# Kernel tuning notes

Hardware: AMD Instinct MI355X
Metric: run time of the kernel (lower is better)

## Reference

```python
import jax, jax.numpy as jnp
import numpy as np

N, C, H, K = 4096, 512, 128, 3
NEG = -jnp.inf


def _linear(x, W, b):
    return x @ W.T + b


def _lrelu(x):
    return jnp.where(x > 0, x, 0.01 * x)  # nn.LeakyReLU default slope


def _cos_sim(x, y):
    # torch cal_cos_similarity: xy / (|x| |y|^T), NaN (0/0) -> 0
    xy = x @ y.T
    den = jnp.linalg.norm(x, axis=1, keepdims=True) * jnp.linalg.norm(y, axis=1, keepdims=True).T
    return xy / jnp.where(den == 0, 1.0, den)


def setup_inputs() -> dict:
    key = jax.random.key(0)
    ks = jax.random.split(key, 24)
    x_hidden = jax.random.normal(ks[0], (N, H), jnp.float32)
    cm = (jax.random.uniform(ks[1], (N, C)) < 0.05).astype(jnp.float32)
    # ensure every concept has at least one member stock (no empty concepts)
    cm = cm.at[jnp.arange(C) % N, jnp.arange(C)].set(1.0)
    market_value = jax.random.uniform(ks[2], (N,), jnp.float32, 0.1, 1.0)
    s = 1.0 / np.sqrt(H)
    inp = {"x_hidden": x_hidden, "concept_matrix": cm, "market_value": market_value}
    names = ["ps", "ps_fore", "ps_back", "hs", "hs_fore", "hs_back", "indi"]
    for i, n in enumerate(names):
        inp[f"W_{n}"] = jax.random.uniform(ks[3 + 2 * i], (H, H), jnp.float32, -s, s)
        inp[f"b_{n}"] = jax.random.uniform(ks[4 + 2 * i], (H,), jnp.float32, -s, s)
    inp["W_out"] = jax.random.uniform(ks[20], (1, H), jnp.float32, -s, s)
    inp["b_out"] = jax.random.uniform(ks[21], (1,), jnp.float32, -s, s)
    return inp


def reference(x_hidden, concept_matrix, market_value,
              W_ps, b_ps, W_ps_fore, b_ps_fore, W_ps_back, b_ps_back,
              W_hs, b_hs, W_hs_fore, b_hs_fore, W_hs_back, b_hs_back,
              W_indi, b_indi, W_out, b_out):
    x = x_hidden
    n = x.shape[0]
    # --- predefined-concept (ps) branch ---
    s2c = concept_matrix * market_value[:, None]                     # [N,C]
    s2c_den = s2c.sum(0)[None, :] * concept_matrix + 1.0
    s2c = s2c / s2c_den
    hidden = s2c.T @ x                                               # [C,H]
    valid1 = hidden.sum(1) != 0                                      # row-filter mask
    s2c2 = jax.nn.softmax(x @ hidden.T, axis=0)                      # softmax over stocks
    hidden = (s2c2.T @ x) * valid1[:, None]                          # [C,H]
    c2s = jax.nn.softmax(jnp.where(valid1[None, :], _cos_sim(x, hidden), NEG), axis=1)
    p_shared = _linear(c2s @ hidden, W_ps, b_ps)
    p_back = _linear(p_shared, W_ps_back, b_ps_back)
    out_ps = _lrelu(_linear(p_shared, W_ps_fore, b_ps_fore))
    # --- hidden-concept (hs) branch ---
    h = x - p_back
    hs2c = _cos_sim(h, h)                                            # [N,N]
    diag = jnp.diagonal(hs2c)
    hs2c = hs2c * (1.0 - jnp.eye(n, dtype=h.dtype))
    idx = jax.lax.top_k(hs2c, K)[1]                                  # [N,K]
    mask = jnp.zeros((n, n), h.dtype).at[jnp.arange(n)[:, None], idx].set(1.0)
    hs2c = hs2c * mask
    hs2c = hs2c + jnp.diag((hs2c.sum(0) != 0).astype(h.dtype) * diag)
    hidden2 = hs2c.T @ h                                             # [N,H]
    valid2 = hidden2.sum(1) != 0
    hidden2 = hidden2 * valid2[:, None]
    hc2s = jax.nn.softmax(jnp.where(valid2[None, :], _cos_sim(h, hidden2), NEG), axis=1)
    h_shared = _linear(hc2s @ hidden2, W_hs, b_hs)
    h_back = _linear(h_shared, W_hs_back, b_hs_back)
    out_hs = _lrelu(_linear(h_shared, W_hs_fore, b_hs_fore))
    # --- individual branch ---
    indiv = x - p_back - h_back
    out_indi = _lrelu(_linear(indiv, W_indi, b_indi))
    all_info = out_ps + out_hs + out_indi
    return _linear(all_info, W_out, b_out).squeeze()                 # [N]
```

## Files before the change

### kernel.cpp

```cpp
#include <hip/hip_runtime.h>
#include <hip/hip_fp16.h>
#include <math.h>

#define N 4096
#define C 512
#define H 128
#define PAD 40

typedef __attribute__((ext_vector_type(8))) short bf16x8;
typedef __attribute__((ext_vector_type(4))) float f32x4;


__device__ inline float wave_reduce_sum(float v) {
#pragma unroll
  for (int m = 32; m; m >>= 1) v += __shfl_xor(v, m);
  return v;
}

__device__ inline float lrelu(float v) { return v > 0.f ? v : 0.01f * v; }

__device__ inline bool better(float v, int j, float w, int k) {
  return (v > w) || (v == w && j < k);
}

__device__ inline void top3_ins(float v, int j, float& v0, int& j0,
                                float& v1, int& j1, float& v2, int& j2) {
  if (better(v, j, v0, j0)) { v2 = v1; j2 = j1; v1 = v0; j1 = j0; v0 = v; j0 = j; }
  else if (better(v, j, v1, j1)) { v2 = v1; j2 = j1; v1 = v; j1 = j; }
  else if (better(v, j, v2, j2)) { v2 = v; j2 = j; }
}

__device__ inline void ins5(float s, int j, float v[5], int jx[5]) {
  if (!better(s, j, v[4], jx[4])) return;
  if (better(s, j, v[0], jx[0])) {
    v[4]=v[3]; jx[4]=jx[3]; v[3]=v[2]; jx[3]=jx[2]; v[2]=v[1]; jx[2]=jx[1];
    v[1]=v[0]; jx[1]=jx[0]; v[0]=s; jx[0]=j;
  } else if (better(s, j, v[1], jx[1])) {
    v[4]=v[3]; jx[4]=jx[3]; v[3]=v[2]; jx[3]=jx[2]; v[2]=v[1]; jx[2]=jx[1];
    v[1]=s; jx[1]=j;
  } else if (better(s, j, v[2], jx[2])) {
    v[4]=v[3]; jx[4]=jx[3]; v[3]=v[2]; jx[3]=jx[2]; v[2]=s; jx[2]=j;
  } else if (better(s, j, v[3], jx[3])) {
    v[4]=v[3]; jx[4]=jx[3]; v[3]=s; jx[3]=j;
  } else {
    v[4]=s; jx[4]=j;
  }
}

__device__ inline unsigned short f2bf(float f) {
  unsigned u = __float_as_uint(f);
  unsigned r = u + 0x7fffu + ((u >> 16) & 1u);
  return (unsigned short)(r >> 16);
}
__device__ inline float bf2f(unsigned short h) {
  return __uint_as_float(((unsigned)h) << 16);
}

__global__ __launch_bounds__(256) void k_split(const float* __restrict__ in,
                                               unsigned short* __restrict__ hi,
                                               unsigned short* __restrict__ lo) {
  int idx = (blockIdx.x * 256 + threadIdx.x) * 4;
  float4 v = *(const float4*)&in[idx];
  float vv[4] = {v.x, v.y, v.z, v.w};
  unsigned short h[4], l[4];
#pragma unroll
  for (int c = 0; c < 4; c++) {
    h[c] = f2bf(vv[c]);
    l[c] = f2bf(vv[c] - bf2f(h[c]));
  }
  uint2 ph = {(unsigned)h[0] | ((unsigned)h[1] << 16),
              (unsigned)h[2] | ((unsigned)h[3] << 16)};
  uint2 pl = {(unsigned)l[0] | ((unsigned)l[1] << 16),
              (unsigned)l[2] | ((unsigned)l[3] << 16)};
  *(uint2*)&hi[idx] = ph;
  *(uint2*)&lo[idx] = pl;
}

__global__ __launch_bounds__(256) void k_tsplit(const float* __restrict__ in,
                                                unsigned short* __restrict__ thi,
                                                unsigned short* __restrict__ tlo,
                                                int R) {
  __shared__ float tile[32][132];
  int r0 = blockIdx.x * 32, tid = threadIdx.x;
#pragma unroll
  for (int q = 0; q < 4; q++) {
    int f = q * 256 + tid;
    int row = f >> 5, ch = f & 31;
    *(float4*)&tile[row][ch * 4] = *(const float4*)&in[(size_t)(r0 + row) * 128 + ch * 4];
  }
  __syncthreads();
  int c = tid & 127, half = tid >> 7;
  unsigned short hh[16], ll[16];
#pragma unroll
  for (int rr = 0; rr < 16; rr++) {
    float v = tile[half * 16 + rr][c];
    hh[rr] = f2bf(v);
    ll[rr] = f2bf(v - bf2f(hh[rr]));
  }
  size_t off = (size_t)c * R + r0 + half * 16;
  uint4 ph0 = {(unsigned)hh[0] | ((unsigned)hh[1] << 16), (unsigned)hh[2] | ((unsigned)hh[3] << 16),
               (unsigned)hh[4] | ((unsigned)hh[5] << 16), (unsigned)hh[6] | ((unsigned)hh[7] << 16)};
  uint4 ph1 = {(unsigned)hh[8] | ((unsigned)hh[9] << 16), (unsigned)hh[10] | ((unsigned)hh[11] << 16),
               (unsigned)hh[12] | ((unsigned)hh[13] << 16), (unsigned)hh[14] | ((unsigned)hh[15] << 16)};
  uint4 pl0 = {(unsigned)ll[0] | ((unsigned)ll[1] << 16), (unsigned)ll[2] | ((unsigned)ll[3] << 16),
               (unsigned)ll[4] | ((unsigned)ll[5] << 16), (unsigned)ll[6] | ((unsigned)ll[7] << 16)};
  uint4 pl1 = {(unsigned)ll[8] | ((unsigned)ll[9] << 16), (unsigned)ll[10] | ((unsigned)ll[11] << 16),
               (unsigned)ll[12] | ((unsigned)ll[13] << 16), (unsigned)ll[14] | ((unsigned)ll[15] << 16)};
  *(uint4*)&thi[off] = ph0; *(uint4*)&thi[off + 8] = ph1;
  *(uint4*)&tlo[off] = pl0; *(uint4*)&tlo[off + 8] = pl1;
}


__global__ __launch_bounds__(64) void k_colsum_s2c(
    const float* __restrict__ cm, const float* __restrict__ mv,
    float* __restrict__ colsum_c) {
  int c = blockIdx.x * 64 + threadIdx.x;
  int i0 = blockIdx.y * 256;
  float acc = 0.f;
  for (int i = i0; i < i0 + 256; i++) acc += cm[(size_t)i * C + c] * mv[i];
  atomicAdd(&colsum_c[c], acc);
}

__global__ __launch_bounds__(64) void k_valid1(const float* __restrict__ hid,
                                               float* __restrict__ valid1) {
  int c = blockIdx.x, t = threadIdx.x;
  float s = hid[(size_t)c * H + t] + hid[(size_t)c * H + 64 + t];
  s = wave_reduce_sum(s);
  if (t == 0) valid1[c] = (s != 0.f) ? 1.f : 0.f;
}

__global__ __launch_bounds__(64) void k_rownorm128(const float* __restrict__ A,
                                                   float* __restrict__ nrm) {
  int r = blockIdx.x, t = threadIdx.x;
  float a = A[(size_t)r * H + t], b = A[(size_t)r * H + 64 + t];
  float ss = wave_reduce_sum(a * a + b * b);
  if (t == 0) nrm[r] = sqrtf(ss);
}

__global__ __launch_bounds__(256) void k_colstats(const float* __restrict__ sc,
                                                  float* __restrict__ colmax,
                                                  float* __restrict__ colsum) {
  __shared__ float red[256];
  int c = blockIdx.x, t = threadIdx.x;
  float v[16];
  float m = -3e38f;
#pragma unroll
  for (int q = 0; q < 16; q++) {
    v[q] = sc[(size_t)(q * 256 + t) * C + c];
    m = fmaxf(m, v[q]);
  }
  red[t] = m; __syncthreads();
  for (int s = 128; s; s >>= 1) { if (t < s) red[t] = fmaxf(red[t], red[t + s]); __syncthreads(); }
  m = red[0]; __syncthreads();
  float sum = 0.f;
#pragma unroll
  for (int q = 0; q < 16; q++) sum += __expf(v[q] - m);
  red[t] = sum; __syncthreads();
  for (int s = 128; s; s >>= 1) { if (t < s) red[t] += red[t + s]; __syncthreads(); }
  if (t == 0) { colmax[c] = m; colsum[c] = red[0]; }
}

__global__ __launch_bounds__(256) void k_cs_softmax(
    const float* __restrict__ sc, const float* __restrict__ xnorm,
    const float* __restrict__ hnorm, const float* __restrict__ valid1,
    unsigned short* __restrict__ cshi, unsigned short* __restrict__ cslo) {
  __shared__ float red[256];
  int i = blockIdx.x, t = threadIdx.x;
  float xn = xnorm[i];
  float r0 = sc[(size_t)i * C + t], r1 = sc[(size_t)i * C + 256 + t];
  float d0 = xn * hnorm[t], d1 = xn * hnorm[256 + t];
  float c0 = r0 / (d0 == 0.f ? 1.f : d0);
  float c1 = r1 / (d1 == 0.f ? 1.f : d1);
  float s0 = (valid1[t] != 0.f) ? c0 : -3e38f;
  float s1 = (valid1[256 + t] != 0.f) ? c1 : -3e38f;
  red[t] = fmaxf(s0, s1); __syncthreads();
  for (int s = 128; s; s >>= 1) { if (t < s) red[t] = fmaxf(red[t], red[t + s]); __syncthreads(); }
  float m = red[0]; __syncthreads();
  float p0 = (s0 > -1e37f) ? __expf(s0 - m) : 0.f;
  float p1 = (s1 > -1e37f) ? __expf(s1 - m) : 0.f;
  red[t] = p0 + p1; __syncthreads();
  for (int s = 128; s; s >>= 1) { if (t < s) red[t] += red[t + s]; __syncthreads(); }
  float inv = 1.f / red[0];
  float a = p0 * inv, b = p1 * inv;
  unsigned short ha = f2bf(a), hb = f2bf(b);
  cshi[(size_t)i * C + t] = ha;
  cslo[(size_t)i * C + t] = f2bf(a - bf2f(ha));
  cshi[(size_t)i * C + 256 + t] = hb;
  cslo[(size_t)i * C + 256 + t] = f2bf(b - bf2f(hb));
}

__global__ __launch_bounds__(64) void k_hhat(const float* __restrict__ h,
                                             float* __restrict__ hhat,
                                             unsigned short* __restrict__ hhi,
                                             unsigned short* __restrict__ hlo,
                                             float* __restrict__ diagv) {
  int i = blockIdx.x, t = threadIdx.x;
  float a = h[(size_t)i * H + t], b = h[(size_t)i * H + 64 + t];
  float ss = wave_reduce_sum(a * a + b * b);
  float hn = sqrtf(ss);
  float den = hn * hn;
  float dg = (den == 0.f) ? 0.f : ss / den;
  float inv = (ss > 0.f) ? (1.f / hn) : 1.f;
  float va = a * inv, vb = b * inv;
  hhat[(size_t)i * H + t] = va;
  hhat[(size_t)i * H + 64 + t] = vb;
  unsigned short ha = f2bf(va), hb = f2bf(vb);
  hhi[(size_t)i * H + t] = ha;
  hlo[(size_t)i * H + t] = f2bf(va - bf2f(ha));
  hhi[(size_t)i * H + 64 + t] = hb;
  hlo[(size_t)i * H + 64 + t] = f2bf(vb - bf2f(hb));
  if (t == 0) diagv[i] = dg;
}

__global__ __launch_bounds__(64) void k_fin_hidden2(
    const float* __restrict__ h, const float* __restrict__ diagv,
    const float* __restrict__ colsum_m, float* __restrict__ hidden2,
    unsigned short* __restrict__ h2hi, unsigned short* __restrict__ h2lo,
    float* __restrict__ valid2f) {
  int j = blockIdx.x, t = threadIdx.x;
  float add = (colsum_m[j] != 0.f) ? diagv[j] : 0.f;
  float a = hidden2[(size_t)j * H + t] + add * h[(size_t)j * H + t];
  float b = hidden2[(size_t)j * H + 64 + t] + add * h[(size_t)j * H + 64 + t];
  float s = a + b, ss = a * a + b * b;
#pragma unroll
  for (int m = 32; m; m >>= 1) { s += __shfl_xor(s, m); ss += __shfl_xor(ss, m); }
  bool valid = (s != 0.f);
  a = valid ? a : 0.f; b = valid ? b : 0.f;
  hidden2[(size_t)j * H + t] = a;
  hidden2[(size_t)j * H + 64 + t] = b;
  float inv = (valid && ss > 0.f) ? (1.f / sqrtf(ss)) : 1.f;
  float va = a * inv, vb = b * inv;
  unsigned short ha = f2bf(va), hb = f2bf(vb);
  h2hi[(size_t)j * H + t] = ha;
  h2lo[(size_t)j * H + t] = f2bf(va - bf2f(ha));
  h2hi[(size_t)j * H + 64 + t] = hb;
  h2lo[(size_t)j * H + 64 + t] = f2bf(vb - bf2f(hb));
  if (t == 0) valid2f[j] = valid ? 1.f : 0.f;
}

__global__ __launch_bounds__(64) void k_final(const float* __restrict__ ai,
                                              const float* __restrict__ Wout,
                                              const float* __restrict__ bout,
// ... 44 lines not shown
#pragma unroll
    for (int t = 0; t < 4; t++) {
      int ar = (wm + t * 16 + l15) * PAD + quad * 8;
      ah[t] = *(const bf16x8*)&sAh[ar];
      al[t] = *(const bf16x8*)&sAl[ar];
      int br = (wn + t * 16 + l15) * PAD + quad * 8;
      bh[t] = *(const bf16x8*)&sBh[br];
      bl[t] = *(const bf16x8*)&sBl[br];
    }
#pragma unroll
    for (int mt = 0; mt < 4; mt++)
#pragma unroll
      for (int nt = 0; nt < 4; nt++) {
        acc[mt][nt] = __builtin_amdgcn_mfma_f32_16x16x32_bf16(ah[mt], bh[nt], acc[mt][nt], 0, 0, 0);
        acc[mt][nt] = __builtin_amdgcn_mfma_f32_16x16x32_bf16(ah[mt], bl[nt], acc[mt][nt], 0, 0, 0);
        acc[mt][nt] = __builtin_amdgcn_mfma_f32_16x16x32_bf16(al[mt], bh[nt], acc[mt][nt], 0, 0, 0);
      }
    __syncthreads();
  }
  if (EPI == 3) {
    float vm[4];
#pragma unroll
    for (int nt = 0; nt < 4; nt++) vm[nt] = validn[bn + wn + nt * 16 + l15];
#pragma unroll
    for (int mt = 0; mt < 4; mt++) {
#pragma unroll
      for (int rg = 0; rg < 4; rg++) {
        int row = bm + wm + mt * 16 + quad * 4 + rg;
        float rsum = 0.f;
#pragma unroll
        for (int nt = 0; nt < 4; nt++) {
          int col = bn + wn + nt * 16 + l15;
          float e = (vm[nt] != 0.f) ? __expf(acc[mt][nt][rg] - 1.f) : 0.f;
          rsum += e;
          ehi[(size_t)row * N + col] = f2bf(e);
        }
#pragma unroll
        for (int d = 1; d < 16; d <<= 1) rsum += __shfl_xor(rsum, d);
        if (l15 == 0) atomicAdd(&lsum[row], rsum);
      }
    }
  } else if (EPI == 2) {
#pragma unroll
    for (int mt = 0; mt < 4; mt++) {
#pragma unroll
      for (int nt = 0; nt < 4; nt++) {
        int col = bn + wn + nt * 16 + l15;
#pragma unroll
        for (int rg = 0; rg < 4; rg++) {
          int row = bm + wm + mt * 16 + quad * 4 + rg;
          float v = (row == col) ? 0.f : acc[mt][nt][rg];
          ehi[(size_t)row * N + col] = __half_as_ushort(__float2half(v));
        }
      }
    }
  } else {
#pragma unroll
    for (int mt = 0; mt < 4; mt++) {
#pragma unroll
      for (int nt = 0; nt < 4; nt++) {
        int col = bn + wn + nt * 16 + l15;
#pragma unroll
        for (int rg = 0; rg < 4; rg++) {
          int row = bm + wm + mt * 16 + quad * 4 + rg;
          out[(size_t)row * Nn + col] = acc[mt][nt][rg];
        }
      }
    }
  }
}

__global__ __launch_bounds__(256) void k_rowtop(
    const unsigned short* __restrict__ Sh, const float* __restrict__ hhat,
    float* __restrict__ mtv, int* __restrict__ mtj) {
  int i = blockIdx.x * 4 + (threadIdx.x >> 6);
  int lane = threadIdx.x & 63;
  const unsigned short* row = &Sh[(size_t)i * N];
  float v[5] = {-3e38f, -3e38f, -3e38f, -3e38f, -3e38f};
  int jx[5] = {0x7fffffff, 0x7fffffff, 0x7fffffff, 0x7fffffff, 0x7fffffff};
  for (int t = 0; t < 8; t++) {
    int base = t * 512 + lane * 8;
    uint4 p = *(const uint4*)&row[base];
    unsigned pk[4] = {p.x, p.y, p.z, p.w};
#pragma unroll
    for (int c = 0; c < 4; c++) {
      float e0 = __half2float(__ushort_as_half((unsigned short)(pk[c] & 0xffffu)));
      float e1 = __half2float(__ushort_as_half((unsigned short)(pk[c] >> 16)));
      ins5(e0, base + c * 2, v, jx);
      ins5(e1, base + c * 2 + 1, v, jx);
    }
  }
#pragma unroll
  for (int d = 1; d < 64; d <<= 1) {
    float fv[5]; int fj[5];
#pragma unroll
    for (int c = 0; c < 5; c++) { fv[c] = __shfl_xor(v[c], d); fj[c] = __shfl_xor(jx[c], d); }
#pragma unroll
    for (int c = 0; c < 5; c++) ins5(fv[c], fj[c], v, jx);
  }
  const float* hi = &hhat[(size_t)i * H];
  float b0 = -3e38f, b1 = -3e38f, b2 = -3e38f;
  int q0 = 0, q1 = 0, q2 = 0;
#pragma unroll
  for (int c = 0; c < 5; c++) {
    int j = jx[c];
    float s;
    if (j == i) {
      s = 0.f;
    } else {
      const float* hj = &hhat[(size_t)j * H];
      float p = hi[lane] * hj[lane] + hi[lane + 64] * hj[lane + 64];
      s = wave_reduce_sum(p);
    }
    top3_ins(s, j, b0, q0, b1, q1, b2, q2);
  }
  if (lane == 0) {
    mtv[i * 3 + 0] = b0; mtv[i * 3 + 1] = b1; mtv[i * 3 + 2] = b2;
    mtj[i * 3 + 0] = q0; mtj[i * 3 + 1] = q1; mtj[i * 3 + 2] = q2;
  }
}

template <int ALO>
__global__ __launch_bounds__(256) void k_mfma_kn(
    const unsigned short* __restrict__ Ahi, const unsigned short* __restrict__ Alo,
    const unsigned short* __restrict__ Bthi, const unsigned short* __restrict__ Btlo,
    float* __restrict__ partial, int lda, int KC) {
  __shared__ __align__(16) unsigned short sAh[128 * PAD];
  __shared__ __align__(16) unsigned short sAl[128 * PAD];
  __shared__ __align__(16) unsigned short sBh[128 * PAD];
  __shared__ __align__(16) unsigned short sBl[128 * PAD];
  int tid = threadIdx.x;
  int bm = blockIdx.y * 128;
  int k0 = blockIdx.z * KC;
  int lane = tid & 63, w = tid >> 6;
  int wm = (w & 1) * 64, wn = (w >> 1) * 64;
  int l15 = lane & 15, quad = lane >> 4;
  f32x4 zero = {0.f, 0.f, 0.f, 0.f};
  f32x4 acc[4][4];
#pragma unroll
  for (int mt = 0; mt < 4; mt++)
#pragma unroll
    for (int nt = 0; nt < 4; nt++) acc[mt][nt] = zero;

  for (int kt = 0; kt < KC; kt += 32) {
#pragma unroll
    for (int q = 0; q < 2; q++) {
      int f = tid * 2 + q;
      int row = f >> 2, ch = f & 3;
      size_t ga = (size_t)(bm + row) * lda + k0 + kt + ch * 8;
      size_t gb = (size_t)row * lda + k0 + kt + ch * 8;
      int ls = row * PAD + ch * 8;
      *(uint4*)&sAh[ls] = *(const uint4*)&Ahi[ga];
      if (ALO) *(uint4*)&sAl[ls] = *(const uint4*)&Alo[ga];
      *(uint4*)&sBh[ls] = *(const uint4*)&Bthi[gb];
      *(uint4*)&sBl[ls] = *(const uint4*)&Btlo[gb];
    }
    __syncthreads();
    bf16x8 ah[4], al[4], bh[4], bl[4];
#pragma unroll
    for (int t = 0; t < 4; t++) {
      int ar = (wm + t * 16 + l15) * PAD + quad * 8;
      ah[t] = *(const bf16x8*)&sAh[ar];
      if (ALO) al[t] = *(const bf16x8*)&sAl[ar];
      int br = (wn + t * 16 + l15) * PAD + quad * 8;
      bh[t] = *(const bf16x8*)&sBh[br];
      bl[t] = *(const bf16x8*)&sBl[br];
    }
#pragma unroll
    for (int mt = 0; mt < 4; mt++)
#pragma unroll
      for (int nt = 0; nt < 4; nt++) {
        acc[mt][nt] = __builtin_amdgcn_mfma_f32_16x16x32_bf16(ah[mt], bh[nt], acc[mt][nt], 0, 0, 0);
        acc[mt][nt] = __builtin_amdgcn_mfma_f32_16x16x32_bf16(ah[mt], bl[nt], acc[mt][nt], 0, 0, 0);
        if (ALO)
          acc[mt][nt] = __builtin_amdgcn_mfma_f32_16x16x32_bf16(al[mt], bh[nt], acc[mt][nt], 0, 0, 0);
      }
    __syncthreads();
  }
  float* pp = partial + (size_t)blockIdx.z * N * 128;
#pragma unroll
  for (int mt = 0; mt < 4; mt++)
#pragma unroll
    for (int nt = 0; nt < 4; nt++) {
      int col = wn + nt * 16 + l15;
#pragma unroll
      for (int rg = 0; rg < 4; rg++) {
        int row = bm + wm + mt * 16 + quad * 4 + rg;
        pp[(size_t)row * 128 + col] = acc[mt][nt][rg];
      }
    }
}

template <int AMODE>
__global__ __launch_bounds__(256) void k_mfma_genA(
    const float* __restrict__ P, const float* __restrict__ mv,
    const float* __restrict__ col1, const float* __restrict__ col2,
    const unsigned short* __restrict__ Bthi, const unsigned short* __restrict__ Btlo,
    float* __restrict__ partial, int KC) {
  __shared__ __align__(16) unsigned short sAh[128 * PAD];
  __shared__ __align__(16) unsigned short sAl[128 * PAD];
  __shared__ __align__(16) unsigned short sBh[128 * PAD];
  __shared__ __align__(16) unsigned short sBl[128 * PAD];
  int tid = threadIdx.x;
  int bm = blockIdx.y * 128;
  int k0 = blockIdx.z * KC;
  int lane = tid & 63, w = tid >> 6;
  int wm = (w & 1) * 64, wn = (w >> 1) * 64;
  int l15 = lane & 15, quad = lane >> 4;
  f32x4 zero = {0.f, 0.f, 0.f, 0.f};
  f32x4 acc[4][4];
#pragma unroll
  for (int mt = 0; mt < 4; mt++)
#pragma unroll
    for (int nt = 0; nt < 4; nt++) acc[mt][nt] = zero;

  for (int kt = 0; kt < KC; kt += 32) {
    int kr = tid >> 3;
    int mc = (tid & 7) * 16;
    int k = k0 + kt + kr;
    float mvk = (AMODE == 1) ? mv[k] : 0.f;
#pragma unroll
    for (int q = 0; q < 4; q++) {
      int m0 = mc + q * 4;
      float4 pv = *(const float4*)&P[(size_t)k * C + bm + m0];
      float4 c1 = *(const float4*)&col1[bm + m0];
      float wv[4];
      if (AMODE == 1) {
        wv[0] = pv.x * mvk / (c1.x * pv.x + 1.f);
        wv[1] = pv.y * mvk / (c1.y * pv.y + 1.f);
        wv[2] = pv.z * mvk / (c1.z * pv.z + 1.f);
        wv[3] = pv.w * mvk / (c1.w * pv.w + 1.f);
      } else {
        float4 c2 = *(const float4*)&col2[bm + m0];
        wv[0] = __expf(pv.x - c1.x) / c2.x;
        wv[1] = __expf(pv.y - c1.y) / c2.y;
        wv[2] = __expf(pv.z - c1.z) / c2.z;
        wv[3] = __expf(pv.w - c1.w) / c2.w;
      }
#pragma unroll
      for (int j = 0; j < 4; j++) {
        unsigned short hh = f2bf(wv[j]);
        sAh[(m0 + j) * PAD + kr] = hh;
        sAl[(m0 + j) * PAD + kr] = f2bf(wv[j] - bf2f(hh));
      }
    }
#pragma unroll
    for (int q = 0; q < 2; q++) {
      int f = q * 256 + tid;
      int row = f >> 2, ch = f & 3;
      size_t gb = (size_t)row * N + k0 + kt + ch * 8;
      int ls = row * PAD + ch * 8;
      *(uint4*)&sBh[ls] = *(const uint4*)&Bthi[gb];
      *(uint4*)&sBl[ls] = *(const uint4*)&Btlo[gb];
    }
    __syncthreads();
    bf16x8 ah[4], al[4], bh[4], bl[4];
#pragma unroll
    for (int t = 0; t < 4; t++) {
      int ar = (wm + t * 16 + l15) * PAD + quad * 8;
      ah[t] = *(const bf16x8*)&sAh[ar];
      al[t] = *(const bf16x8*)&sAl[ar];
      int br = (wn + t * 16 + l15) * PAD + quad * 8;
      bh[t] = *(const bf16x8*)&sBh[br];
      bl[t] = *(const bf16x8*)&sBl[br];
    }
#pragma unroll
    for (int mt = 0; mt < 4; mt++)
#pragma unroll
      for (int nt = 0; nt < 4; nt++) {
        acc[mt][nt] = __builtin_amdgcn_mfma_f32_16x16x32_bf16(ah[mt], bh[nt], acc[mt][nt], 0, 0, 0);
        acc[mt][nt] = __builtin_amdgcn_mfma_f32_16x16x32_bf16(ah[mt], bl[nt], acc[mt][nt], 0, 0, 0);
        acc[mt][nt] = __builtin_amdgcn_mfma_f32_16x16x32_bf16(al[mt], bh[nt], acc[mt][nt], 0, 0, 0);
      }
    __syncthreads();
  }
  float* pp = partial + (size_t)blockIdx.z * C * 128;
#pragma unroll
  for (int mt = 0; mt < 4; mt++)
#pragma unroll
    for (int nt = 0; nt < 4; nt++) {
      int col = wn + nt * 16 + l15;
#pragma unroll
      for (int rg = 0; rg < 4; rg++) {
        int row = bm + wm + mt * 16 + quad * 4 + rg;
        pp[(size_t)row * 128 + col] = acc[mt][nt][rg];
      }
    }
}

template <int EPI>
__global__ __launch_bounds__(256) void k_mfma_lin(
    const float* __restrict__ A, const float* __restrict__ Wt,
    const float* __restrict__ bias, const float* __restrict__ aux,
    float* __restrict__ out) {
  __shared__ __align__(16) unsigned short sAh[32 * PAD];
  __shared__ __align__(16) unsigned short sAl[32 * PAD];
  __shared__ __align__(16) unsigned short sWh[128 * PAD];
  __shared__ __align__(16) unsigned short sWl[128 * PAD];
  int tid = threadIdx.x;
  int bm = blockIdx.y * 32;
  int lane = tid & 63, w = tid >> 6;
  int rt = (w & 1) * 16, ch2 = (w >> 1) * 64;
  int l15 = lane & 15, quad = lane >> 4;
  f32x4 zero = {0.f, 0.f, 0.f, 0.f};
  f32x4 acc[4];
#pragma unroll
  for (int nt = 0; nt < 4; nt++) acc[nt] = zero;

  for (int kt = 0; kt < 128; kt += 32) {
    {
      int arow = tid >> 3, ach = tid & 7;
      float4 av = *(const float4*)&A[(size_t)(bm + arow) * 128 + kt + ach * 4];
      float aa[4] = {av.x, av.y, av.z, av.w};
      int ls = arow * PAD + ach * 4;
#pragma unroll
      for (int c = 0; c < 4; c++) {
        unsigned short hh = f2bf(aa[c]);
        sAh[ls + c] = hh;
        sAl[ls + c] = f2bf(aa[c] - bf2f(hh));
      }
    }
#pragma unroll
    for (int q = 0; q < 4; q++) {
      int f = q * 256 + tid;
      int wrow = f >> 3, wch = f & 7;
      float4 wv = *(const float4*)&Wt[(size_t)wrow * 128 + kt + wch * 4];
      float ww[4] = {wv.x, wv.y, wv.z, wv.w};
      int ls = wrow * PAD + wch * 4;
#pragma unroll
      for (int c = 0; c < 4; c++) {
        unsigned short hh = f2bf(ww[c]);
        sWh[ls + c] = hh;
        sWl[ls + c] = f2bf(ww[c] - bf2f(hh));
      }
    }
    __syncthreads();
    bf16x8 ah, al, bh[4], bl[4];
    {
      int ar = (rt + l15) * PAD + quad * 8;
      ah = *(const bf16x8*)&sAh[ar];
      al = *(const bf16x8*)&sAl[ar];
    }
#pragma unroll
    for (int nt = 0; nt < 4; nt++) {
      int br = (ch2 + nt * 16 + l15) * PAD + quad * 8;
      bh[nt] = *(const bf16x8*)&sWh[br];
      bl[nt] = *(const bf16x8*)&sWl[br];
    }
#pragma unroll
    for (int nt = 0; nt < 4; nt++) {
      acc[nt] = __builtin_amdgcn_mfma_f32_16x16x32_bf16(ah, bh[nt], acc[nt], 0, 0, 0);
      acc[nt] = __builtin_amdgcn_mfma_f32_16x16x32_bf16(ah, bl[nt], acc[nt], 0, 0, 0);
      acc[nt] = __builtin_amdgcn_mfma_f32_16x16x32_bf16(al, bh[nt], acc[nt], 0, 0, 0);
    }
    __syncthreads();
  }
#pragma unroll
  for (int nt = 0; nt < 4; nt++) {
    int col = ch2 + nt * 16 + l15;
    float bv = bias[col];
#pragma unroll
    for (int rg = 0; rg < 4; rg++) {
      int row = bm + rt + quad * 4 + rg;
      size_t off = (size_t)row * 128 + col;
      float v = acc[nt][rg] + bv;
      if (EPI == 0) out[off] = v;
      else if (EPI == 1) out[off] = lrelu(v);
      else if (EPI == 2) out[off] += lrelu(v);
      else out[off] = aux[off] - v;
    }
  }
}

__global__ __launch_bounds__(256) void k_scatter(
    const float* __restrict__ mtv, const int* __restrict__ mtj,
    const float* __restrict__ h, float* __restrict__ hidden2,
    float* __restrict__ colsum_m) {
  int i = blockIdx.x * 4 + (threadIdx.x >> 6);
  int lane = threadIdx.x & 63;
  float h0 = h[(size_t)i * H + lane], h1 = h[(size_t)i * H + 64 + lane];
#pragma unroll
  for (int s = 0; s < 3; s++) {
    float v = mtv[i * 3 + s];
    int j = mtj[i * 3 + s];
    atomicAdd(&hidden2[(size_t)j * H + lane], v * h0);
    atomicAdd(&hidden2[(size_t)j * H + 64 + lane], v * h1);
    if (lane == s) atomicAdd(&colsum_m[j], v);
  }
}

__global__ __launch_bounds__(256) void k_reduce(
    const float* __restrict__ partial, float* __restrict__ out, int cnt,
    size_t slot, size_t size4, const float* __restrict__ scalem,
    const float* __restrict__ divm, unsigned short* __restrict__ hi,
    unsigned short* __restrict__ lo) {
  size_t idx = (size_t)blockIdx.x * 256 + threadIdx.x;
  if (idx >= size4) return;
  float4 s = {0, 0, 0, 0};
  for (int c = 0; c < cnt; c++) {
    float4 v = *(const float4*)&partial[c * slot + idx * 4];
    s.x += v.x; s.y += v.y; s.z += v.z; s.w += v.w;
  }
  if (scalem) {
    float sc = scalem[idx >> 5];
    s.x *= sc; s.y *= sc; s.z *= sc; s.w *= sc;
  }
  if (divm) {
    float sc = 1.f / divm[idx >> 5];
    s.x *= sc; s.y *= sc; s.z *= sc; s.w *= sc;
  }
  *(float4*)&out[idx * 4] = s;
  if (hi) {
    float vv[4] = {s.x, s.y, s.z, s.w};
    unsigned short h[4], l[4];
#pragma unroll
    for (int c = 0; c < 4; c++) {
      h[c] = f2bf(vv[c]);
      l[c] = f2bf(vv[c] - bf2f(h[c]));
    }
    uint2 ph = {(unsigned)h[0] | ((unsigned)h[1] << 16),
                (unsigned)h[2] | ((unsigned)h[3] << 16)};
    uint2 pl = {(unsigned)l[0] | ((unsigned)l[1] << 16),
                (unsigned)l[2] | ((unsigned)l[3] << 16)};
    *(uint2*)&hi[idx * 4] = ph;
    *(uint2*)&lo[idx * 4] = pl;
  }
}


extern "C" void kernel_launch(void* const* d_in, const int* in_sizes, int n_in,
                              void* d_out, int out_size, void* d_ws, size_t ws_size,
                              hipStream_t stream) {
  (void)in_sizes; (void)n_in; (void)out_size;
  const float* x   = (const float*)d_in[0];
  const float* cm  = (const float*)d_in[1];
  const float* mv  = (const float*)d_in[2];
  const float* W_ps = (const float*)d_in[3],  *b_ps = (const float*)d_in[4];
  const float* W_psf = (const float*)d_in[5], *b_psf = (const float*)d_in[6];
  const float* W_psb = (const float*)d_in[7], *b_psb = (const float*)d_in[8];
  const float* W_hs = (const float*)d_in[9],  *b_hs = (const float*)d_in[10];
  const float* W_hsf = (const float*)d_in[11], *b_hsf = (const float*)d_in[12];
  const float* W_hsb = (const float*)d_in[13], *b_hsb = (const float*)d_in[14];
  const float* W_in = (const float*)d_in[15], *b_in = (const float*)d_in[16];
  const float* W_out = (const float*)d_in[17], *b_out = (const float*)d_in[18];
  float* out = (float*)d_out;

  float* W = (float*)d_ws;
  size_t o = 0;
  auto alloc = [&](size_t n) { float* p = W + o; o += n; return p; };
  float* colsum_c = alloc(C);
  float* colmax   = alloc(C);
  float* colsumexp= alloc(C);
  float* valid1   = alloc(C);
  float* hnorm_ps = alloc(C);
  float* xnorm    = alloc(N);
  float* diagv    = alloc(N);
  float* colsum_m = alloc(N);
  float* valid2f  = alloc(N);
  float* lsum     = alloc(N);
  float* mtv      = alloc(3 * N);
  int*   mtj      = (int*)alloc(3 * N);
  float* hidden1  = alloc((size_t)C * H);
  float* hidden_ps= alloc((size_t)C * H);
  float* scores   = alloc((size_t)N * C);
  float* ps_pre   = alloc((size_t)N * H);
  float* p_shared = alloc((size_t)N * H);
  float* all_info = alloc((size_t)N * H);
  float* hbuf     = alloc((size_t)N * H);
  float* hhat     = alloc((size_t)N * H);
  float* hidden2  = alloc((size_t)N * H);
  unsigned short* xhi    = (unsigned short*)alloc((size_t)N * H / 2);
  unsigned short* xlo    = (unsigned short*)alloc((size_t)N * H / 2);
  unsigned short* hhathi = (unsigned short*)alloc((size_t)N * H / 2);
  unsigned short* hhatlo = (unsigned short*)alloc((size_t)N * H / 2);
  unsigned short* h2hi   = (unsigned short*)alloc((size_t)N * H / 2);
  unsigned short* h2lo   = (unsigned short*)alloc((size_t)N * H / 2);
  unsigned short* h1hi   = (unsigned short*)alloc((size_t)C * H / 2);
  unsigned short* h1lo   = (unsigned short*)alloc((size_t)C * H / 2);
  unsigned short* hpshi  = (unsigned short*)alloc((size_t)C * H / 2);
  unsigned short* hpslo  = (unsigned short*)alloc((size_t)C * H / 2);
  unsigned short* cshi   = (unsigned short*)alloc((size_t)N * C / 2);
  unsigned short* cslo   = (unsigned short*)alloc((size_t)N * C / 2);
  unsigned short* hpst_hi= (unsigned short*)alloc((size_t)H * C / 2);
  unsigned short* hpst_lo= (unsigned short*)alloc((size_t)H * C / 2);
  unsigned short* h2t_hi = (unsigned short*)alloc((size_t)H * N / 2);
  unsigned short* h2t_lo = (unsigned short*)alloc((size_t)H * N / 2);
  unsigned short* xt_hi  = (unsigned short*)alloc((size_t)H * N / 2);
  unsigned short* xt_lo  = (unsigned short*)alloc((size_t)H * N / 2);
  float* Sbuf     = alloc((size_t)N * N / 2);
  unsigned short* Sh  = (unsigned short*)Sbuf;
  unsigned short* Ehi = (unsigned short*)Sbuf;
  float* partial  = W + o;
  size_t rem = ws_size / 4 - o;
  int Z = (rem >= (size_t)16 * N * H) ? 16 : 8;
  int KC = 4096 / Z;

  hipMemsetAsync(colsum_c, 0, C * sizeof(float), stream);
  hipMemsetAsync(colsum_m, 0, N * sizeof(float), stream);
  hipMemsetAsync(lsum, 0, N * sizeof(float), stream);
  hipMemsetAsync(hidden2, 0, (size_t)N * H * sizeof(float), stream);

  dim3 blk(256);
  k_split<<<dim3(N * H / 1024), blk, 0, stream>>>(x, xhi, xlo);
  k_tsplit<<<dim3(N / 32), blk, 0, stream>>>(x, xt_hi, xt_lo, N);
  k_colsum_s2c<<<dim3(C / 64, 16), dim3(64), 0, stream>>>(cm, mv, colsum_c);
  k_mfma_genA<1><<<dim3(1, C / 128, 32), blk, 0, stream>>>(
      cm, mv, colsum_c, nullptr, xt_hi, xt_lo, partial, N / 32);
  k_reduce<<<dim3(C * H / 4 / 256), blk, 0, stream>>>(
      partial, hidden1, 32, (size_t)C * H, (size_t)C * H / 4, nullptr, nullptr,
      h1hi, h1lo);
  k_valid1<<<dim3(C), dim3(64), 0, stream>>>(hidden1, valid1);
  k_mfma_nt<0><<<dim3(C / 128, N / 128), blk, 0, stream>>>(
      xhi, xlo, h1hi, h1lo, nullptr, scores, nullptr, nullptr, C);
  k_colstats<<<dim3(C), blk, 0, stream>>>(scores, colmax, colsumexp);
  k_mfma_genA<2><<<dim3(1, C / 128, 32), blk, 0, stream>>>(
      scores, nullptr, colmax, colsumexp, xt_hi, xt_lo, partial, N / 32);
  k_reduce<<<dim3(C * H / 4 / 256), blk, 0, stream>>>(
      partial, hidden_ps, 32, (size_t)C * H, (size_t)C * H / 4, valid1, nullptr,
      hpshi, hpslo);
  k_rownorm128<<<dim3(N), dim3(64), 0, stream>>>(x, xnorm);
  k_rownorm128<<<dim3(C), dim3(64), 0, stream>>>(hidden_ps, hnorm_ps);
  k_mfma_nt<0><<<dim3(C / 128, N / 128), blk, 0, stream>>>(
      xhi, xlo, hpshi, hpslo, nullptr, scores, nullptr, nullptr, C);
  k_cs_softmax<<<dim3(N), blk, 0, stream>>>(scores, xnorm, hnorm_ps, valid1,
                                            cshi, cslo);
  k_tsplit<<<dim3(C / 32), blk, 0, stream>>>(hidden_ps, hpst_hi, hpst_lo, C);
  k_mfma_kn<1><<<dim3(1, N / 128, 4), blk, 0, stream>>>(
      cshi, cslo, hpst_hi, hpst_lo, partial, C, C / 4);
  k_reduce<<<dim3(N * H / 4 / 256), blk, 0, stream>>>(
      partial, ps_pre, 4, (size_t)N * H, (size_t)N * H / 4, nullptr, nullptr,
      nullptr, nullptr);
  k_mfma_lin<0><<<dim3(1, N / 32), blk, 0, stream>>>(
      ps_pre, W_ps, b_ps, nullptr, p_shared);
  k_mfma_lin<3><<<dim3(1, N / 32), blk, 0, stream>>>(
      p_shared, W_psb, b_psb, x, hbuf);
  k_mfma_lin<1><<<dim3(1, N / 32), blk, 0, stream>>>(
      p_shared, W_psf, b_psf, nullptr, all_info);
  k_hhat<<<dim3(N), dim3(64), 0, stream>>>(hbuf, hhat, hhathi, hhatlo, diagv);
  k_mfma_nt<2><<<dim3(N / 128, N / 128), blk, 0, stream>>>(
      hhathi, hhatlo, hhathi, hhatlo, nullptr, nullptr, Sh, nullptr, N);
  k_rowtop<<<dim3(N / 4), blk, 0, stream>>>(Sh, hhat, mtv, mtj);
  k_scatter<<<dim3(N / 4), blk, 0, stream>>>(mtv, mtj, hbuf, hidden2, colsum_m);
  k_fin_hidden2<<<dim3(N), dim3(64), 0, stream>>>(hbuf, diagv, colsum_m, hidden2,
                                                  h2hi, h2lo, valid2f);
  k_mfma_nt<3><<<dim3(N / 128, N / 128), blk, 0, stream>>>(
      hhathi, hhatlo, h2hi, h2lo, valid2f, nullptr, Ehi, lsum, N);
  k_tsplit<<<dim3(N / 32), blk, 0, stream>>>(hidden2, h2t_hi, h2t_lo, N);
  k_mfma_kn<0><<<dim3(1, N / 128, Z), blk, 0, stream>>>(
      Ehi, nullptr, h2t_hi, h2t_lo, partial, N, KC);
  k_reduce<<<dim3(N * H / 4 / 256), blk, 0, stream>>>(
      partial, ps_pre, Z, (size_t)N * H, (size_t)N * H / 4, nullptr, lsum,
      nullptr, nullptr);
  k_mfma_lin<0><<<dim3(1, N / 32), blk, 0, stream>>>(
      ps_pre, W_hs, b_hs, nullptr, p_shared);
  k_mfma_lin<2><<<dim3(1, N / 32), blk, 0, stream>>>(
      p_shared, W_hsf, b_hsf, nullptr, all_info);
  k_mfma_lin<3><<<dim3(1, N / 32), blk, 0, stream>>>(
      p_shared, W_hsb, b_hsb, hbuf, hbuf);
  k_mfma_lin<2><<<dim3(1, N / 32), blk, 0, stream>>>(
      hbuf, W_in, b_in, nullptr, all_info);
  k_final<<<dim3(N), dim3(64), 0, stream>>>(all_info, W_out, b_out, out);
}
```

Measured before the change: 415.4 us.

## Replace split-K partial buffers with atomic accumulation and fuse paired linears

Split-K GEMM kernels now atomically add into the output instead of writing per-slice partials, so the separate k_reduce passes go away. Their scaling and bf16 split steps move into the consumers (the valid mask into genA, the lsum divide into the linear, k_split for hi/lo). Column softmax stats become two row-parallel kernels using atomicMax on an order-preserving float key, plus atomicAdd for the sums. Pairs of linears sharing an input are fused into one kernel, and the row top-k scan skips 8-element chunks that cannot enter the top five. Atomics make the summation order nondeterministic, and more memsets are added.

```diff
diff --git a/kernel.cpp b/kernel.cpp
--- a/kernel.cpp
+++ b/kernel.cpp
@@ -56,6 +56,15 @@
   return __uint_as_float(((unsigned)h) << 16);
 }
 
+__device__ inline unsigned fkey(float f) {
+  unsigned u = __float_as_uint(f);
+  return (u & 0x80000000u) ? ~u : (u | 0x80000000u);
+}
+__device__ inline float fkey_dec(unsigned k) {
+  unsigned u = (k & 0x80000000u) ? (k ^ 0x80000000u) : ~k;
+  return __uint_as_float(u);
+}
+
 __global__ __launch_bounds__(256) void k_split(const float* __restrict__ in,
                                                unsigned short* __restrict__ hi,
                                                unsigned short* __restrict__ lo) {
@@ -137,27 +146,35 @@
   if (t == 0) nrm[r] = sqrtf(ss);
 }
 
-__global__ __launch_bounds__(256) void k_colstats(const float* __restrict__ sc,
-                                                  float* __restrict__ colmax,
-                                                  float* __restrict__ colsum) {
-  __shared__ float red[256];
-  int c = blockIdx.x, t = threadIdx.x;
-  float v[16];
-  float m = -3e38f;
-#pragma unroll
-  for (int q = 0; q < 16; q++) {
-    v[q] = sc[(size_t)(q * 256 + t) * C + c];
-    m = fmaxf(m, v[q]);
-  }
-  red[t] = m; __syncthreads();
-  for (int s = 128; s; s >>= 1) { if (t < s) red[t] = fmaxf(red[t], red[t + s]); __syncthreads(); }
-  m = red[0]; __syncthreads();
-  float sum = 0.f;
-#pragma unroll
-  for (int q = 0; q < 16; q++) sum += __expf(v[q] - m);
-  red[t] = sum; __syncthreads();
-  for (int s = 128; s; s >>= 1) { if (t < s) red[t] += red[t + s]; __syncthreads(); }
-  if (t == 0) { colmax[c] = m; colsum[c] = red[0]; }
+__global__ __launch_bounds__(256) void k_colmax(const float* __restrict__ sc,
+                                                unsigned* __restrict__ colmax_u) {
+  int r0 = blockIdx.x * 64, tid = threadIdx.x;
+  int c0 = tid, c1 = tid + 256;
+  float m0 = -3e38f, m1 = -3e38f;
+  for (int r = 0; r < 64; r++) {
+    const float* row = &sc[(size_t)(r0 + r) * C];
+    m0 = fmaxf(m0, row[c0]);
+    m1 = fmaxf(m1, row[c1]);
+  }
+  atomicMax(&colmax_u[c0], fkey(m0));
+  atomicMax(&colmax_u[c1], fkey(m1));
+}
+
+__global__ __launch_bounds__(256) void k_colsumexp(
+    const float* __restrict__ sc, const unsigned* __restrict__ colmax_u,
+    float* __restrict__ colmax_f, float* __restrict__ colsum) {
+  int r0 = blockIdx.x * 64, tid = threadIdx.x;
+  int c0 = tid, c1 = tid + 256;
+  float m0 = fkey_dec(colmax_u[c0]), m1 = fkey_dec(colmax_u[c1]);
+  if (blockIdx.x == 0) { colmax_f[c0] = m0; colmax_f[c1] = m1; }
+  float s0 = 0.f, s1 = 0.f;
+  for (int r = 0; r < 64; r++) {
+    const float* row = &sc[(size_t)(r0 + r) * C];
+    s0 += __expf(row[c0] - m0);
+    s1 += __expf(row[c1] - m1);
+  }
+  atomicAdd(&colsum[c0], s0);
+  atomicAdd(&colsum[c1], s1);
 }
 
 __global__ __launch_bounds__(256) void k_cs_softmax(
@@ -368,13 +385,17 @@
     int base = t * 512 + lane * 8;
     uint4 p = *(const uint4*)&row[base];
     unsigned pk[4] = {p.x, p.y, p.z, p.w};
+    float e[8];
 #pragma unroll
     for (int c = 0; c < 4; c++) {
-      float e0 = __half2float(__ushort_as_half((unsigned short)(pk[c] & 0xffffu)));
-      float e1 = __half2float(__ushort_as_half((unsigned short)(pk[c] >> 16)));
-      ins5(e0, base + c * 2, v, jx);
-      ins5(e1, base + c * 2 + 1, v, jx);
-    }
+      e[c * 2] = __half2float(__ushort_as_half((unsigned short)(pk[c] & 0xffffu)));
+      e[c * 2 + 1] = __half2float(__ushort_as_half((unsigned short)(pk[c] >> 16)));
+    }
+    float mx = fmaxf(fmaxf(fmaxf(e[0], e[1]), fmaxf(e[2], e[3])),
+                     fmaxf(fmaxf(e[4], e[5]), fmaxf(e[6], e[7])));
+    if (!better(mx, base, v[4], jx[4])) continue;
+#pragma unroll
+    for (int c = 0; c < 8; c++) ins5(e[c], base + c, v, jx);
   }
 #pragma unroll
   for (int d = 1; d < 64; d <<= 1) {
@@ -410,7 +431,7 @@
 __global__ __launch_bounds__(256) void k_mfma_kn(
     const unsigned short* __restrict__ Ahi, const unsigned short* __restrict__ Alo,
     const unsigned short* __restrict__ Bthi, const unsigned short* __restrict__ Btlo,
-    float* __restrict__ partial, int lda, int KC) {
+    float* __restrict__ out, int lda, int KC) {
   __shared__ __align__(16) unsigned short sAh[128 * PAD];
   __shared__ __align__(16) unsigned short sAl[128 * PAD];
   __shared__ __align__(16) unsigned short sBh[128 * PAD];
@@ -463,7 +484,6 @@
       }
     __syncthreads();
   }
-  float* pp = partial + (size_t)blockIdx.z * N * 128;
 #pragma unroll
   for (int mt = 0; mt < 4; mt++)
 #pragma unroll
@@ -472,7 +492,7 @@
 #pragma unroll
       for (int rg = 0; rg < 4; rg++) {
         int row = bm + wm + mt * 16 + quad * 4 + rg;
-        pp[(size_t)row * 128 + col] = acc[mt][nt][rg];
+        atomicAdd(&out[(size_t)row * 128 + col], acc[mt][nt][rg]);
       }
     }
 }
@@ -481,8 +501,9 @@
 __global__ __launch_bounds__(256) void k_mfma_genA(
     const float* __restrict__ P, const float* __restrict__ mv,
     const float* __restrict__ col1, const float* __restrict__ col2,
+    const float* __restrict__ validm,
     const unsigned short* __restrict__ Bthi, const unsigned short* __restrict__ Btlo,
-    float* __restrict__ partial, int KC) {
+    float* __restrict__ out, int KC) {
   __shared__ __align__(16) unsigned short sAh[128 * PAD];
   __shared__ __align__(16) unsigned short sAl[128 * PAD];
   __shared__ __align__(16) unsigned short sBh[128 * PAD];
@@ -518,10 +539,11 @@
         wv[3] = pv.w * mvk / (c1.w * pv.w + 1.f);
       } else {
         float4 c2 = *(const float4*)&col2[bm + m0];
-        wv[0] = __expf(pv.x - c1.x) / c2.x;
-        wv[1] = __expf(pv.y - c1.y) / c2.y;
-        wv[2] = __expf(pv.z - c1.z) / c2.z;
-        wv[3] = __expf(pv.w - c1.w) / c2.w;
+        float4 vv = *(const float4*)&validm[bm + m0];
+        wv[0] = __expf(pv.x - c1.x) / c2.x * vv.x;
+        wv[1] = __expf(pv.y - c1.y) / c2.y * vv.y;
+        wv[2] = __expf(pv.z - c1.z) / c2.z * vv.z;
+        wv[3] = __expf(pv.w - c1.w) / c2.w * vv.w;
       }
 #pragma unroll
       for (int j = 0; j < 4; j++) {
@@ -560,7 +582,6 @@
       }
     __syncthreads();
   }
-  float* pp = partial + (size_t)blockIdx.z * C * 128;
 #pragma unroll
   for (int mt = 0; mt < 4; mt++)
 #pragma unroll
@@ -569,7 +590,7 @@
 #pragma unroll
       for (int rg = 0; rg < 4; rg++) {
         int row = bm + wm + mt * 16 + quad * 4 + rg;
-        pp[(size_t)row * 128 + col] = acc[mt][nt][rg];
+        atomicAdd(&out[(size_t)row * 128 + col], acc[mt][nt][rg]);
       }
     }
 }
@@ -578,7 +599,7 @@
 __global__ __launch_bounds__(256) void k_mfma_lin(
     const float* __restrict__ A, const float* __restrict__ Wt,
     const float* __restrict__ bias, const float* __restrict__ aux,
-    float* __restrict__ out) {
+    float* __restrict__ out, const float* __restrict__ divm) {
   __shared__ __align__(16) unsigned short sAh[32 * PAD];
   __shared__ __align__(16) unsigned short sAl[32 * PAD];
   __shared__ __align__(16) unsigned short sWh[128 * PAD];
@@ -588,6 +609,7 @@
   int lane = tid & 63, w = tid >> 6;
   int rt = (w & 1) * 16, ch2 = (w >> 1) * 64;
   int l15 = lane & 15, quad = lane >> 4;
+  float ascale = divm ? (1.f / divm[bm + (tid >> 3)]) : 1.f;
   f32x4 zero = {0.f, 0.f, 0.f, 0.f};
   f32x4 acc[4];
 #pragma unroll
@@ -597,7 +619,7 @@
     {
       int arow = tid >> 3, ach = tid & 7;
       float4 av = *(const float4*)&A[(size_t)(bm + arow) * 128 + kt + ach * 4];
-      float aa[4] = {av.x, av.y, av.z, av.w};
+      float aa[4] = {av.x * ascale, av.y * ascale, av.z * ascale, av.w * ascale};
       int ls = arow * PAD + ach * 4;
 #pragma unroll
       for (int c = 0; c < 4; c++) {
@@ -658,6 +680,109 @@
   }
 }
 
+template <int E1, int E2>
+__global__ __launch_bounds__(256) void k_mfma_lin2(
+    const float* __restrict__ A,
+    const float* __restrict__ W1, const float* __restrict__ b1,
+    const float* __restrict__ aux1, float* __restrict__ out1,
+    const float* __restrict__ W2, const float* __restrict__ b2,
+    const float* __restrict__ aux2, float* __restrict__ out2) {
+  __shared__ __align__(16) unsigned short sAh[32 * PAD];
+  __shared__ __align__(16) unsigned short sAl[32 * PAD];
+  __shared__ __align__(16) unsigned short sW1h[128 * PAD];
+  __shared__ __align__(16) unsigned short sW1l[128 * PAD];
+  __shared__ __align__(16) unsigned short sW2h[128 * PAD];
+  __shared__ __align__(16) unsigned short sW2l[128 * PAD];
+  int tid = threadIdx.x;
+  int bm = blockIdx.y * 32;
+  int lane = tid & 63, w = tid >> 6;
+  int rt = (w & 1) * 16, ch2 = (w >> 1) * 64;
+  int l15 = lane & 15, quad = lane >> 4;
+  f32x4 zero = {0.f, 0.f, 0.f, 0.f};
+  f32x4 acc1[4], acc2[4];
+#pragma unroll
+  for (int nt = 0; nt < 4; nt++) { acc1[nt] = zero; acc2[nt] = zero; }
+
+  for (int kt = 0; kt < 128; kt += 32) {
+    {
+      int arow = tid >> 3, ach = tid & 7;
+      float4 av = *(const float4*)&A[(size_t)(bm + arow) * 128 + kt + ach * 4];
+      float aa[4] = {av.x, av.y, av.z, av.w};
+      int ls = arow * PAD + ach * 4;
+#pragma unroll
+      for (int c = 0; c < 4; c++) {
+        unsigned short hh = f2bf(aa[c]);
+        sAh[ls + c] = hh;
+        sAl[ls + c] = f2bf(aa[c] - bf2f(hh));
+      }
+    }
+#pragma unroll
+    for (int q = 0; q < 4; q++) {
+      int f = q * 256 + tid;
+      int wrow = f >> 3, wch = f & 7;
+      int ls = wrow * PAD + wch * 4;
+      float4 wv = *(const float4*)&W1[(size_t)wrow * 128 + kt + wch * 4];
+      float ww[4] = {wv.x, wv.y, wv.z, wv.w};
+#pragma unroll
+      for (int c = 0; c < 4; c++) {
+        unsigned short hh = f2bf(ww[c]);
+        sW1h[ls + c] = hh;
+        sW1l[ls + c] = f2bf(ww[c] - bf2f(hh));
+      }
+      float4 wv2 = *(const float4*)&W2[(size_t)wrow * 128 + kt + wch * 4];
+      float ww2[4] = {wv2.x, wv2.y, wv2.z, wv2.w};
+#pragma unroll
+      for (int c = 0; c < 4; c++) {
+        unsigned short hh = f2bf(ww2[c]);
+        sW2h[ls + c] = hh;
+        sW2l[ls + c] = f2bf(ww2[c] - bf2f(hh));
+      }
+    }
+    __syncthreads();
+    bf16x8 ah, al;
+    {
+      int ar = (rt + l15) * PAD + quad * 8;
+      ah = *(const bf16x8*)&sAh[ar];
+      al = *(const bf16x8*)&sAl[ar];
+    }
+#pragma unroll
+    for (int nt = 0; nt < 4; nt++) {
+      int br = (ch2 + nt * 16 + l15) * PAD + quad * 8;
+      bf16x8 b1h = *(const bf16x8*)&sW1h[br];
+      bf16x8 b1l = *(const bf16x8*)&sW1l[br];
+      bf16x8 b2h = *(const bf16x8*)&sW2h[br];
+      bf16x8 b2l = *(const bf16x8*)&sW2l[br];
+      acc1[nt] = __builtin_amdgcn_mfma_f32_16x16x32_bf16(ah, b1h, acc1[nt], 0, 0, 0);
+      acc1[nt] = __builtin_amdgcn_mfma_f32_16x16x32_bf16(ah, b1l, acc1[nt], 0, 0, 0);
+      acc1[nt] = __builtin_amdgcn_mfma_f32_16x16x32_bf16(al, b1h, acc1[nt], 0, 0, 0);
+      acc2[nt] = __builtin_amdgcn_mfma_f32_16x16x32_bf16(ah, b2h, acc2[nt], 0, 0, 0);
+      acc2[nt] = __builtin_amdgcn_mfma_f32_16x16x32_bf16(ah, b2l, acc2[nt], 0, 0, 0);
+      acc2[nt] = __builtin_amdgcn_mfma_f32_16x16x32_bf16(al, b2h, acc2[nt], 0, 0, 0);
+    }
+    __syncthreads();
+  }
+#pragma unroll
+  for (int nt = 0; nt < 4; nt++) {
+    int col = ch2 + nt * 16 + l15;
+    float bv1 = b1[col], bv2 = b2[col];
+#pragma unroll
+    for (int rg = 0; rg < 4; rg++) {
+      int row = bm + rt + quad * 4 + rg;
+      size_t off = (size_t)row * 128 + col;
+      float v1 = acc1[nt][rg] + bv1;
+      if (E1 == 0) out1[off] = v1;
+      else if (E1 == 1) out1[off] = lrelu(v1);
+      else if (E1 == 2) out1[off] += lrelu(v1);
+      else out1[off] = aux1[off] - v1;
+      float v2 = acc2[nt][rg] + bv2;
+      if (E2 == 0) out2[off] = v2;
+      else if (E2 == 1) out2[off] = lrelu(v2);
+      else if (E2 == 2) out2[off] += lrelu(v2);
+      else out2[off] = aux2[off] - v2;
+    }
+  }
+}
+
 __global__ __launch_bounds__(256) void k_scatter(
     const float* __restrict__ mtv, const int* __restrict__ mtj,
     const float* __restrict__ h, float* __restrict__ hidden2,
@@ -675,49 +800,11 @@
   }
 }
 
-__global__ __launch_bounds__(256) void k_reduce(
-    const float* __restrict__ partial, float* __restrict__ out, int cnt,
-    size_t slot, size_t size4, const float* __restrict__ scalem,
-    const float* __restrict__ divm, unsigned short* __restrict__ hi,
-    unsigned short* __restrict__ lo) {
-  size_t idx = (size_t)blockIdx.x * 256 + threadIdx.x;
-  if (idx >= size4) return;
-  float4 s = {0, 0, 0, 0};
-  for (int c = 0; c < cnt; c++) {
-    float4 v = *(const float4*)&partial[c * slot + idx * 4];
-    s.x += v.x; s.y += v.y; s.z += v.z; s.w += v.w;
-  }
-  if (scalem) {
-    float sc = scalem[idx >> 5];
-    s.x *= sc; s.y *= sc; s.z *= sc; s.w *= sc;
-  }
-  if (divm) {
-    float sc = 1.f / divm[idx >> 5];
-    s.x *= sc; s.y *= sc; s.z *= sc; s.w *= sc;
-  }
-  *(float4*)&out[idx * 4] = s;
-  if (hi) {
-    float vv[4] = {s.x, s.y, s.z, s.w};
-    unsigned short h[4], l[4];
-#pragma unroll
-    for (int c = 0; c < 4; c++) {
-      h[c] = f2bf(vv[c]);
-      l[c] = f2bf(vv[c] - bf2f(h[c]));
-    }
-    uint2 ph = {(unsigned)h[0] | ((unsigned)h[1] << 16),
-                (unsigned)h[2] | ((unsigned)h[3] << 16)};
-    uint2 pl = {(unsigned)l[0] | ((unsigned)l[1] << 16),
-                (unsigned)l[2] | ((unsigned)l[3] << 16)};
-    *(uint2*)&hi[idx * 4] = ph;
-    *(uint2*)&lo[idx * 4] = pl;
-  }
-}
-
 
 extern "C" void kernel_launch(void* const* d_in, const int* in_sizes, int n_in,
                               void* d_out, int out_size, void* d_ws, size_t ws_size,
                               hipStream_t stream) {
-  (void)in_sizes; (void)n_in; (void)out_size;
+  (void)in_sizes; (void)n_in; (void)out_size; (void)ws_size;
   const float* x   = (const float*)d_in[0];
   const float* cm  = (const float*)d_in[1];
   const float* mv  = (const float*)d_in[2];
@@ -735,7 +822,8 @@
   size_t o = 0;
   auto alloc = [&](size_t n) { float* p = W + o; o += n; return p; };
   float* colsum_c = alloc(C);
-  float* colmax   = alloc(C);
+  unsigned* colmaxu = (unsigned*)alloc(C);
+  float* colmaxf  = alloc(C);
   float* colsumexp= alloc(C);
   float* valid1   = alloc(C);
   float* hnorm_ps = alloc(C);
@@ -776,14 +864,15 @@
   float* Sbuf     = alloc((size_t)N * N / 2);
   unsigned short* Sh  = (unsigned short*)Sbuf;
   unsigned short* Ehi = (unsigned short*)Sbuf;
-  float* partial  = W + o;
-  size_t rem = ws_size / 4 - o;
-  int Z = (rem >= (size_t)16 * N * H) ? 16 : 8;
-  int KC = 4096 / Z;
 
   hipMemsetAsync(colsum_c, 0, C * sizeof(float), stream);
+  hipMemsetAsync(colmaxu, 0, C * sizeof(unsigned), stream);
+  hipMemsetAsync(colsumexp, 0, C * sizeof(float), stream);
   hipMemsetAsync(colsum_m, 0, N * sizeof(float), stream);
   hipMemsetAsync(lsum, 0, N * sizeof(float), stream);
+  hipMemsetAsync(hidden1, 0, (size_t)C * H * sizeof(float), stream);
+  hipMemsetAsync(hidden_ps, 0, (size_t)C * H * sizeof(float), stream);
+  hipMemsetAsync(ps_pre, 0, (size_t)N * H * sizeof(float), stream);
   hipMemsetAsync(hidden2, 0, (size_t)N * H * sizeof(float), stream);
 
   dim3 blk(256);
@@ -791,19 +880,16 @@
   k_tsplit<<<dim3(N / 32), blk, 0, stream>>>(x, xt_hi, xt_lo, N);
   k_colsum_s2c<<<dim3(C / 64, 16), dim3(64), 0, stream>>>(cm, mv, colsum_c);
   k_mfma_genA<1><<<dim3(1, C / 128, 32), blk, 0, stream>>>(
-      cm, mv, colsum_c, nullptr, xt_hi, xt_lo, partial, N / 32);
-  k_reduce<<<dim3(C * H / 4 / 256), blk, 0, stream>>>(
-      partial, hidden1, 32, (size_t)C * H, (size_t)C * H / 4, nullptr, nullptr,
-      h1hi, h1lo);
+      cm, mv, colsum_c, nullptr, nullptr, xt_hi, xt_lo, hidden1, N / 32);
   k_valid1<<<dim3(C), dim3(64), 0, stream>>>(hidden1, valid1);
+  k_split<<<dim3(C * H / 1024), blk, 0, stream>>>(hidden1, h1hi, h1lo);
   k_mfma_nt<0><<<dim3(C / 128, N / 128), blk, 0, stream>>>(
       xhi, xlo, h1hi, h1lo, nullptr, scores, nullptr, nullptr, C);
-  k_colstats<<<dim3(C), blk, 0, stream>>>(scores, colmax, colsumexp);
+  k_colmax<<<dim3(N / 64), blk, 0, stream>>>(scores, colmaxu);
+  k_colsumexp<<<dim3(N / 64), blk, 0, stream>>>(scores, colmaxu, colmaxf, colsumexp);
   k_mfma_genA<2><<<dim3(1, C / 128, 32), blk, 0, stream>>>(
-      scores, nullptr, colmax, colsumexp, xt_hi, xt_lo, partial, N / 32);
-  k_reduce<<<dim3(C * H / 4 / 256), blk, 0, stream>>>(
-      partial, hidden_ps, 32, (size_t)C * H, (size_t)C * H / 4, valid1, nullptr,
-      hpshi, hpslo);
+      scores, nullptr, colmaxf, colsumexp, valid1, xt_hi, xt_lo, hidden_ps, N / 32);
+  k_split<<<dim3(C * H / 1024), blk, 0, stream>>>(hidden_ps, hpshi, hpslo);
   k_rownorm128<<<dim3(N), dim3(64), 0, stream>>>(x, xnorm);
   k_rownorm128<<<dim3(C), dim3(64), 0, stream>>>(hidden_ps, hnorm_ps);
   k_mfma_nt<0><<<dim3(C / 128, N / 128), blk, 0, stream>>>(
@@ -812,16 +898,12 @@
                                             cshi, cslo);
   k_tsplit<<<dim3(C / 32), blk, 0, stream>>>(hidden_ps, hpst_hi, hpst_lo, C);
   k_mfma_kn<1><<<dim3(1, N / 128, 4), blk, 0, stream>>>(
-      cshi, cslo, hpst_hi, hpst_lo, partial, C, C / 4);
-  k_reduce<<<dim3(N * H / 4 / 256), blk, 0, stream>>>(
-      partial, ps_pre, 4, (size_t)N * H, (size_t)N * H / 4, nullptr, nullptr,
-      nullptr, nullptr);
+      cshi, cslo, hpst_hi, hpst_lo, ps_pre, C, C / 4);
   k_mfma_lin<0><<<dim3(1, N / 32), blk, 0, stream>>>(
-      ps_pre, W_ps, b_ps, nullptr, p_shared);
-  k_mfma_lin<3><<<dim3(1, N / 32), blk, 0, stream>>>(
-      p_shared, W_psb, b_psb, x, hbuf);
-  k_mfma_lin<1><<<dim3(1, N / 32), blk, 0, stream>>>(
-      p_shared, W_psf, b_psf, nullptr, all_info);
+      ps_pre, W_ps, b_ps, nullptr, p_shared, nullptr);
+  k_mfma_lin2<3, 1><<<dim3(1, N / 32), blk, 0, stream>>>(
+      p_shared, W_psb, b_psb, x, hbuf,
+      W_psf, b_psf, nullptr, all_info);
   k_hhat<<<dim3(N), dim3(64), 0, stream>>>(hbuf, hhat, hhathi, hhatlo, diagv);
   k_mfma_nt<2><<<dim3(N / 128, N / 128), blk, 0, stream>>>(
       hhathi, hhatlo, hhathi, hhatlo, nullptr, nullptr, Sh, nullptr, N);
@@ -832,18 +914,15 @@
   k_mfma_nt<3><<<dim3(N / 128, N / 128), blk, 0, stream>>>(
       hhathi, hhatlo, h2hi, h2lo, valid2f, nullptr, Ehi, lsum, N);
   k_tsplit<<<dim3(N / 32), blk, 0, stream>>>(hidden2, h2t_hi, h2t_lo, N);
-  k_mfma_kn<0><<<dim3(1, N / 128, Z), blk, 0, stream>>>(
-      Ehi, nullptr, h2t_hi, h2t_lo, partial, N, KC);
-  k_reduce<<<dim3(N * H / 4 / 256), blk, 0, stream>>>(
-      partial, ps_pre, Z, (size_t)N * H, (size_t)N * H / 4, nullptr, lsum,
-      nullptr, nullptr);
+  hipMemsetAsync(ps_pre, 0, (size_t)N * H * sizeof(float), stream);
+  k_mfma_kn<0><<<dim3(1, N / 128, 16), blk, 0, stream>>>(
+      Ehi, nullptr, h2t_hi, h2t_lo, ps_pre, N, N / 16);
   k_mfma_lin<0><<<dim3(1, N / 32), blk, 0, stream>>>(
-      ps_pre, W_hs, b_hs, nullptr, p_shared);
+      ps_pre, W_hs, b_hs, nullptr, p_shared, lsum);
+  k_mfma_lin2<2, 3><<<dim3(1, N / 32), blk, 0, stream>>>(
+      p_shared, W_hsf, b_hsf, nullptr, all_info,
+      W_hsb, b_hsb, hbuf, hbuf);
   k_mfma_lin<2><<<dim3(1, N / 32), blk, 0, stream>>>(
-      p_shared, W_hsf, b_hsf, nullptr, all_info);
-  k_mfma_lin<3><<<dim3(1, N / 32), blk, 0, stream>>>(
-      p_shared, W_hsb, b_hsb, hbuf, hbuf);
-  k_mfma_lin<2><<<dim3(1, N / 32), blk, 0, stream>>>(
-      hbuf, W_in, b_in, nullptr, all_info);
+      hbuf, W_in, b_in, nullptr, all_info, nullptr);
   k_final<<<dim3(N), dim3(64), 0, stream>>>(all_info, W_out, b_out, out);
 }
```

After: 444.1 us. +6.9%, slower.
